# Kernel optimization log

Measured on AMD Instinct MI355X. Metric: run time of the kernel, lower is better.

Reference implementation:

```python
import jax, jax.numpy as jnp
import numpy as np

E, B, L, H1, H2, C = 8, 4096, 512, 1024, 512, 40


def setup_inputs() -> dict:
    key = jax.random.key(0)
    ks = jax.random.split(key, 9)
    return {
        "x_s": jax.random.normal(ks[0], (B, L), jnp.float32),
        "x_p": jax.random.normal(ks[1], (B, L), jnp.float32),
        "W1": jax.random.normal(ks[2], (E, 2 * L, H1), jnp.float32) / np.sqrt(2 * L).astype(np.float32),
        "b1": jax.random.normal(ks[3], (E, H1), jnp.float32) * 0.01,
        "W2": jax.random.normal(ks[4], (E, H1, H2), jnp.float32) / np.sqrt(H1).astype(np.float32),
        "b2": jax.random.normal(ks[5], (E, H2), jnp.float32) * 0.01,
        "W3": jax.random.normal(ks[6], (E, H2, C), jnp.float32) / np.sqrt(H2).astype(np.float32),
        "b3": jax.random.normal(ks[7], (E, C), jnp.float32) * 0.01,
        "sub_module_label": jax.random.randint(ks[8], (B,), 0, E, dtype=jnp.int32),
        "sub_id": 0,
    }


def reference(x_s, x_p, W1, b1, W2, b2, W3, b3, sub_module_label, sub_id):
    # Encoders (EEGNet/SCN/DCN) abstracted as identity: x_s / x_p are latent features.
    # Cls_HEAD.forward: x = cat([x_p, x_s], dim=1); per-sample routed 3-layer ELU MLP head.
    # Dropout is identity in eval mode.
    x = jnp.concatenate([x_p, x_s], axis=1)                      # [B, 2L]
    h = jax.nn.elu(jnp.einsum('bi,eih->ebh', x, W1) + b1[:, None, :])   # [E, B, H1]
    h = jax.nn.elu(jnp.einsum('ebh,ehk->ebk', h, W2) + b2[:, None, :])  # [E, B, H2]
    out_all = jnp.einsum('ebk,ekc->ebc', h, W3) + b3[:, None, :]        # [E, B, C]
    # select each sample's routed expert output
    bidx = jnp.arange(x.shape[0])
    return out_all[sub_module_label, bidx]                       # [B, C]
```

## Files before the change

kernel.cpp:

```cpp
#include <hip/hip_runtime.h>
#include <hip/hip_bf16.h>
#include <math.h>

#define En   8
#define Bn   4096
#define Ln   512
#define K1n  1024
#define H1n  1024
#define H2n  512
#define Cn   40
#define NP3  48
#define NTR  72

typedef unsigned short u16;
typedef __attribute__((ext_vector_type(8))) short bf16x8;
typedef __attribute__((ext_vector_type(4))) float f32x4;

__device__ __forceinline__ u16 f2b(float f) {
    union { float f; unsigned int u; } v; v.f = f;
    unsigned int r = v.u + 0x7FFF + ((v.u >> 16) & 1);
    return (u16)(r >> 16);
}

__device__ __forceinline__ void g2l16(const void* g, void* l) {
    __builtin_amdgcn_global_load_lds(
        (const __attribute__((address_space(1))) unsigned int*)(unsigned long long)g,
        (__attribute__((address_space(3))) unsigned int*)(unsigned int)(unsigned long long)l,
        16, 0, 0);
}

__device__ __forceinline__ void wtrans64(
    const float* __restrict__ Wsrc, u16* __restrict__ Wdst,
    int K, int N, int k0, int n0, int tid, float* sm )
{
    #pragma unroll
    for (int s = 0; s < 4; s++) {
        int idx = tid + s * 256;
        int kk = idx >> 4, c4 = (idx & 15) * 4;
        float4 v = *(const float4*)&Wsrc[(size_t)(k0 + kk) * N + n0 + c4];
        float* row = sm + kk * 65 + c4;
        row[0] = v.x; row[1] = v.y; row[2] = v.z; row[3] = v.w;
    }
    __syncthreads();
    #pragma unroll
    for (int s = 0; s < 4; s++) {
        int idx = tid + s * 256;
        int nn = idx >> 4, kc = (idx & 15) * 4;
        ushort4 o = make_ushort4(f2b(sm[(kc + 0) * 65 + nn]), f2b(sm[(kc + 1) * 65 + nn]),
                                 f2b(sm[(kc + 2) * 65 + nn]), f2b(sm[(kc + 3) * 65 + nn]));
        *(ushort4*)&Wdst[(size_t)(n0 + nn) * K + k0 + kc] = o;
    }
}

#define P1_TOT (1 + 256 + 2048)

__global__ __launch_bounds__(256) void prep1_kernel(
    const float* __restrict__ xs, const float* __restrict__ xp,
    const float* __restrict__ W1, const int* __restrict__ label,
    int* __restrict__ meta, int* __restrict__ perm,
    u16* __restrict__ Xb, u16* __restrict__ W1t)
{
    __shared__ __align__(16) float sm[64 * 65];
    const int bid = blockIdx.x;
    const int tid = threadIdx.x;

    if (bid == 0) {
        int* cnt = (int*)sm;
        int* off = cnt + En;
        if (tid < En) cnt[tid] = 0;
        __syncthreads();
        for (int b = tid; b < Bn; b += 256) atomicAdd(&cnt[label[b]], 1);
        __syncthreads();
        if (tid == 0) {
            int run = 0;
            for (int e = 0; e < En; e++) { off[e] = run; run += cnt[e]; }
            off[En] = run;
        }
        __syncthreads();
        if (tid < En) cnt[tid] = off[tid];
        __syncthreads();
        for (int b = tid; b < Bn; b += 256) {
            int e = label[b];
            perm[atomicAdd(&cnt[e], 1)] = b;
        }
        if (tid <= En) meta[tid] = off[tid];
    } else if (bid < 257) {
        int r0 = (bid - 1) * 16;
        #pragma unroll 4
        for (int s = 0; s < 16; s++) {
            int r = r0 + s;
            int k = tid * 4;
            const float* src = (k < Ln) ? (xp + (size_t)r * Ln + k)
                                        : (xs + (size_t)r * Ln + (k - Ln));
            float4 v = *(const float4*)src;
            *(ushort4*)&Xb[(size_t)r * K1n + k] =
                make_ushort4(f2b(v.x), f2b(v.y), f2b(v.z), f2b(v.w));
        }
    } else {
        int b = bid - 257;
        int e = b >> 8, rem = b & 255;
        int k0 = (rem >> 4) * 64, n0 = (rem & 15) * 64;
        wtrans64(W1 + (size_t)e * K1n * H1n, W1t + (size_t)e * H1n * K1n,
                 K1n, H1n, k0, n0, tid, sm);
    }
}

template <int K, int N, bool GATHER, bool FUSE3, bool PREP2>
__global__ __launch_bounds__(256) void mfma_gemm(
    const u16* __restrict__ A, const u16* __restrict__ Wt,
    const float* __restrict__ bias, const int* __restrict__ meta,
    const int* __restrict__ perm, u16* __restrict__ outb,
    const u16* __restrict__ Wt3, float* __restrict__ outf,
    const float* __restrict__ W2f, const float* __restrict__ W3f,
    const float* __restrict__ b3v, const int* __restrict__ labelv,
    u16* __restrict__ W2t_o, u16* __restrict__ W3t_o)
{
    constexpr int TM = 64, BK = 64;
    constexpr int T = K / BK;
    constexpr int NTC = N / 64;
    __shared__ __align__(16) u16 SM[16384];

    const int tid = threadIdx.x;
    const int bx = blockIdx.x;

    if (PREP2 && bx >= NTR * NTC) {
        int jb = bx - NTR * NTC;
        if (jb < 1024) {
            int e = jb >> 7, rem = jb & 127;
            int k0 = (rem >> 3) * 64, n0 = (rem & 7) * 64;
            wtrans64(W2f + (size_t)e * H1n * H2n, W2t_o + (size_t)e * H2n * H1n,
                     H1n, H2n, k0, n0, tid, (float*)SM);
        } else if (jb < 1024 + 128) {
            int b = jb - 1024;
            int e = b >> 4, k0 = (b & 15) * 32;
            const float* src = W3f + (size_t)e * H2n * Cn;
            u16* dst = W3t_o + (size_t)e * NP3 * H2n;
            float* t = (float*)SM;
            #pragma unroll
            for (int s = 0; s < 5; s++) {
                int idx = tid + s * 256;
                int kk = idx / Cn, nn = idx - kk * Cn;
                if (kk < 32) t[kk * 41 + nn] = src[(size_t)(k0 + kk) * Cn + nn];
            }
            __syncthreads();
            #pragma unroll
            for (int s = 0; s < 6; s++) {
                int idx = tid + s * 256;
                int nn = idx >> 5, kk = idx & 31;
                float v = (nn < Cn) ? t[kk * 41 + nn] : 0.f;
                dst[(size_t)nn * H2n + k0 + kk] = f2b(v);
            }
        } else {
            int b = jb - (1024 + 128);
            int r0 = b * 64;
            #pragma unroll
            for (int s = 0; s < 10; s++) {
                int idx = tid + s * 256;
                int r = r0 + idx / Cn;
                int c = idx - (idx / Cn) * Cn;
                outf[(size_t)r * Cn + c] = b3v[labelv[r] * Cn + c];
            }
        }
        return;
    }

    const int rt = bx % NTR;
    const int col0 = (bx / NTR) * 64;

    int expert = -1, row0 = 0, rowmax = 0, acc_t = 0;
    int prev = meta[0];
    #pragma unroll
    for (int e = 0; e < En; e++) {
        int nxt = meta[e + 1];
        int c = nxt - prev;
        int t = (c + TM - 1) / TM;
        if (expert < 0 && rt < acc_t + t) {
            expert = e; row0 = prev + (rt - acc_t) * TM; rowmax = nxt - 1;
        }
        acc_t += t; prev = nxt;
    }
    if (expert < 0) return;

    const u16* Wexp = Wt + (size_t)expert * N * K;

    const int lane = tid & 63;
    const int wid = tid >> 6;
    const int wm = (wid & 1) * 32;
    const int wn = (wid >> 1) * 32;
    const int l15 = lane & 15;
    const int lq = lane >> 4;

    const u16* aptr[2]; const u16* bptr[2];
    int aoff[2], boff[2];
    #pragma unroll
    for (int s = 0; s < 2; s++) {
        int idx = tid + s * 256;
        int rl = idx >> 3, c = idx & 7;
        int kq = c ^ (rl & 7);
        int rg = row0 + rl; if (rg > rowmax) rg = rowmax;
        if (GATHER) rg = perm[rg];
        aptr[s] = A + (size_t)rg * K + kq * 8;
        bptr[s] = Wexp + (size_t)(col0 + rl) * K + kq * 8;
        aoff[s] = idx * 8;
        boff[s] = 4096 + idx * 8;
    }
    const int csw = l15 & 7;

    f32x4 acc[2][2];
    #pragma unroll
    for (int i = 0; i < 2; i++)
        #pragma unroll
        for (int j = 0; j < 2; j++) acc[i][j] = (f32x4){0.f, 0.f, 0.f, 0.f};

    #pragma unroll
    for (int s = 0; s < 2; s++) {
        g2l16(aptr[s], &SM[aoff[s]]);
        g2l16(bptr[s], &SM[boff[s]]);
    }

    for (int t = 0; t < T; t++) {
        __syncthreads();
        const u16* As = &SM[(t & 1) * 8192];
        const u16* Bs = As + 4096;
        if (t + 1 < T) {
            int base = ((t + 1) & 1) * 8192;
            int ko = (t + 1) * BK;
            #pragma unroll
            for (int s = 0; s < 2; s++) {
                g2l16(aptr[s] + ko, &SM[base + aoff[s]]);
                g2l16(bptr[s] + ko, &SM[base + boff[s]]);
            }
        }
        #pragma unroll
        for (int h = 0; h < 2; h++) {
            const int ksw = ((h * 4 + lq) ^ csw) << 3;
            bf16x8 af[2], bf[2];
            #pragma unroll
            for (int i = 0; i < 2; i++)
                af[i] = *(const bf16x8*)&As[(wm + i * 16 + l15) * BK + ksw];
            #pragma unroll
            for (int j = 0; j < 2; j++)
                bf[j] = *(const bf16x8*)&Bs[(wn + j * 16 + l15) * BK + ksw];
            #pragma unroll
            for (int i = 0; i < 2; i++)
                #pragma unroll
                for (int j = 0; j < 2; j++)
                    acc[i][j] = __builtin_amdgcn_mfma_f32_16x16x32_bf16(
                        af[i], bf[j], acc[i][j], 0, 0, 0);
        }
    }

    if (!FUSE3) {
        #pragma unroll
        for (int i = 0; i < 2; i++) {
            #pragma unroll
            for (int j = 0; j < 2; j++) {
                int col = col0 + wn + j * 16 + l15;
                float bv = bias[expert * N + col];
                #pragma unroll
                for (int r = 0; r < 4; r++) {
                    int grow = row0 + wm + i * 16 + lq * 4 + r;
                    if (grow <= rowmax) {
                        float v = acc[i][j][r] + bv;
                        v = (v > 0.f) ? v : (expf(v) - 1.f);
                        outb[(size_t)grow * N + col] = f2b(v);
                    }
                }
            }
        }
    } else {
        __syncthreads();
        u16* H = &SM[0];
        #pragma unroll
        for (int i = 0; i < 2; i++) {
            #pragma unroll
            for (int j = 0; j < 2; j++) {
                int col = wn + j * 16 + l15;
                float bv = bias[expert * N + col0 + col];
                #pragma unroll
                for (int r = 0; r < 4; r++) {
                    float v = acc[i][j][r] + bv;
                    v = (v > 0.f) ? v : (expf(v) - 1.f);
                    H[(wm + i * 16 + lq * 4 + r) * 72 + col] = f2b(v);
                }
            }
        }
        __syncthreads();
        const int rh = wid * 16;
        f32x4 a3[3];
        #pragma unroll
        for (int j = 0; j < 3; j++) a3[j] = (f32x4){0.f, 0.f, 0.f, 0.f};
        #pragma unroll
        for (int ki = 0; ki < 2; ki++) {
            bf16x8 ha = *(const bf16x8*)&H[(rh + l15) * 72 + ki * 32 + lq * 8];
            #pragma unroll
            for (int j = 0; j < 3; j++) {
                bf16x8 wb = *(const bf16x8*)
                    &Wt3[((size_t)expert * NP3 + j * 16 + l15) * H2n + col0 + ki * 32 + lq * 8];
                a3[j] = __builtin_amdgcn_mfma_f32_16x16x32_bf16(ha, wb, a3[j], 0, 0, 0);
            }
        }
        #pragma unroll
        for (int j = 0; j < 3; j++) {
            int col = j * 16 + l15;
            if (col < Cn) {
                #pragma unroll
                for (int r = 0; r < 4; r++) {
                    int grow = row0 + rh + lq * 4 + r;
                    if (grow <= rowmax)
                        atomicAdd(&outf[(size_t)perm[grow] * Cn + col], a3[j][r]);
                }
            }
        }
    }
}

extern "C" void kernel_launch(void* const* d_in, const int* in_sizes, int n_in,
                              void* d_out, int out_size, void* d_ws, size_t ws_size,
                              hipStream_t stream)
{
    const float* xs = (const float*)d_in[0];
    const float* xp = (const float*)d_in[1];
    const float* W1 = (const float*)d_in[2];
    const float* b1 = (const float*)d_in[3];
    const float* W2 = (const float*)d_in[4];
    const float* b2 = (const float*)d_in[5];
    const float* W3 = (const float*)d_in[6];
    const float* b3 = (const float*)d_in[7];
    const int* label = (const int*)d_in[8];
    float* out = (float*)d_out;

    char* ws = (char*)d_ws;
    int* meta = (int*)ws;
    int* perm = (int*)(ws + 64);
    u16* Xb  = (u16*)(ws + (64 << 10));
    u16* W1t = (u16*)(ws + (64 << 10) + (8  << 20));
    u16* W2t = (u16*)(ws + (64 << 10) + (24 << 20));
    u16* h1b = (u16*)(ws + (64 << 10) + (32 << 20));
    u16* W3t = (u16*)(ws + (64 << 10) + (40 << 20));

    prep1_kernel<<<P1_TOT, 256, 0, stream>>>(
        xs, xp, W1, label, meta, perm, Xb, W1t);

    mfma_gemm<K1n, H1n, true, false, true><<<72 * 16 + 1216, 256, 0, stream>>>(
        Xb, W1t, b1, meta, perm, h1b, nullptr, out,
        W2, W3, b3, label, W2t, W3t);

    mfma_gemm<H1n, H2n, false, true, false><<<72 * 8, 256, 0, stream>>>(
        h1b, W2t, b2, meta, perm, nullptr, W3t, out,
        nullptr, nullptr, nullptr, nullptr, nullptr, nullptr);
}
```

Before: 172.1 us.

## Fuse fp32-to-bf16 conversion of X and W1 into first GEMM's load path

Removes the separate pass that converted X to bf16 and transposed W1 into bf16 scratch. The first GEMM now reads fp32 X rows (gathered via perm) and fp32 W1 directly, converting to bf16 in registers and writing into swizzled LDS with register prefetch double buffering. Routing becomes its own one-block kernel. This avoids writing and re-reading the bf16 copies. In exchange, each tile re-reads and re-converts the fp32 weights, doubling global bytes for W1 per tile. The synchronous register-staged loads also replace the async LDS loads that the GEMM used before.

Measured after the change: 187.6 us. 1.09x slower.

```diff
diff --git a/kernel.cpp b/kernel.cpp
--- a/kernel.cpp
+++ b/kernel.cpp
@@ -21,6 +21,12 @@
     unsigned int r = v.u + 0x7FFF + ((v.u >> 16) & 1);
     return (u16)(r >> 16);
 }
+__device__ __forceinline__ unsigned int f2b2(float a, float b) {
+    union { float f; unsigned int u; } x, y; x.f = a; y.f = b;
+    unsigned int ra = (x.u + 0x7FFF + ((x.u >> 16) & 1)) >> 16;
+    unsigned int rb = (y.u + 0x7FFF + ((y.u >> 16) & 1)) & 0xFFFF0000u;
+    return rb | ra;
+}
 
 __device__ __forceinline__ void g2l16(const void* g, void* l) {
     __builtin_amdgcn_global_load_lds(
@@ -31,7 +37,7 @@
 
 __device__ __forceinline__ void wtrans64(
     const float* __restrict__ Wsrc, u16* __restrict__ Wdst,
-    int K, int N, int k0, int n0, int tid, float* sm )
+    int K, int N, int k0, int n0, int tid, float* sm)
 {
     #pragma unroll
     for (int s = 0; s < 4; s++) {
@@ -52,78 +58,46 @@
     }
 }
 
-#define P1_TOT (1 + 256 + 2048)
-
-__global__ __launch_bounds__(256) void prep1_kernel(
-    const float* __restrict__ xs, const float* __restrict__ xp,
-    const float* __restrict__ W1, const int* __restrict__ label,
-    int* __restrict__ meta, int* __restrict__ perm,
-    u16* __restrict__ Xb, u16* __restrict__ W1t)
+__global__ __launch_bounds__(256) void route_kernel(
+    const int* __restrict__ label, int* __restrict__ meta, int* __restrict__ perm)
 {
-    __shared__ __align__(16) float sm[64 * 65];
-    const int bid = blockIdx.x;
+    __shared__ int cnt[En], off[En + 1];
     const int tid = threadIdx.x;
-
-    if (bid == 0) {
-        int* cnt = (int*)sm;
-        int* off = cnt + En;
-        if (tid < En) cnt[tid] = 0;
-        __syncthreads();
-        for (int b = tid; b < Bn; b += 256) atomicAdd(&cnt[label[b]], 1);
-        __syncthreads();
-        if (tid == 0) {
-            int run = 0;
-            for (int e = 0; e < En; e++) { off[e] = run; run += cnt[e]; }
-            off[En] = run;
-        }
-        __syncthreads();
-        if (tid < En) cnt[tid] = off[tid];
-        __syncthreads();
-        for (int b = tid; b < Bn; b += 256) {
-            int e = label[b];
-            perm[atomicAdd(&cnt[e], 1)] = b;
-        }
-        if (tid <= En) meta[tid] = off[tid];
-    } else if (bid < 257) {
-        int r0 = (bid - 1) * 16;
-        #pragma unroll 4
-        for (int s = 0; s < 16; s++) {
-            int r = r0 + s;
-            int k = tid * 4;
-            const float* src = (k < Ln) ? (xp + (size_t)r * Ln + k)
-                                        : (xs + (size_t)r * Ln + (k - Ln));
-            float4 v = *(const float4*)src;
-            *(ushort4*)&Xb[(size_t)r * K1n + k] =
-                make_ushort4(f2b(v.x), f2b(v.y), f2b(v.z), f2b(v.w));
-        }
-    } else {
-        int b = bid - 257;
-        int e = b >> 8, rem = b & 255;
-        int k0 = (rem >> 4) * 64, n0 = (rem & 15) * 64;
-        wtrans64(W1 + (size_t)e * K1n * H1n, W1t + (size_t)e * H1n * K1n,
-                 K1n, H1n, k0, n0, tid, sm);
-    }
-}
-
-template <int K, int N, bool GATHER, bool FUSE3, bool PREP2>
-__global__ __launch_bounds__(256) void mfma_gemm(
-    const u16* __restrict__ A, const u16* __restrict__ Wt,
-    const float* __restrict__ bias, const int* __restrict__ meta,
-    const int* __restrict__ perm, u16* __restrict__ outb,
-    const u16* __restrict__ Wt3, float* __restrict__ outf,
+    if (tid < En) cnt[tid] = 0;
+    __syncthreads();
+    for (int b = tid; b < Bn; b += 256) atomicAdd(&cnt[label[b]], 1);
+    __syncthreads();
+    if (tid == 0) {
+        int run = 0;
+        for (int e = 0; e < En; e++) { off[e] = run; run += cnt[e]; }
+        off[En] = run;
+    }
+    __syncthreads();
+    if (tid < En) cnt[tid] = off[tid];
+    __syncthreads();
+    for (int b = tid; b < Bn; b += 256) {
+        int e = label[b];
+        perm[atomicAdd(&cnt[e], 1)] = b;
+    }
+    if (tid <= En) meta[tid] = off[tid];
+}
+
+__global__ __launch_bounds__(256) void gemm1_kernel(
+    const float* __restrict__ xp, const float* __restrict__ xs,
+    const float* __restrict__ W1, const float* __restrict__ b1,
+    const int* __restrict__ meta, const int* __restrict__ perm,
+    u16* __restrict__ h1b,
     const float* __restrict__ W2f, const float* __restrict__ W3f,
     const float* __restrict__ b3v, const int* __restrict__ labelv,
-    u16* __restrict__ W2t_o, u16* __restrict__ W3t_o)
+    u16* __restrict__ W2t_o, u16* __restrict__ W3t_o, float* __restrict__ outf)
 {
-    constexpr int TM = 64, BK = 64;
-    constexpr int T = K / BK;
-    constexpr int NTC = N / 64;
+    constexpr int TM = 64, BK = 64, T = K1n / BK, NTC = H1n / 64;
     __shared__ __align__(16) u16 SM[16384];
 
     const int tid = threadIdx.x;
     const int bx = blockIdx.x;
 
-    if (PREP2 && bx >= NTR * NTC) {
+    if (bx >= NTR * NTC) {
         int jb = bx - NTR * NTC;
         if (jb < 1024) {
             int e = jb >> 7, rem = jb & 127;
@@ -181,8 +155,6 @@
     }
     if (expert < 0) return;
 
-    const u16* Wexp = Wt + (size_t)expert * N * K;
-
     const int lane = tid & 63;
     const int wid = tid >> 6;
     const int wm = (wid & 1) * 32;
@@ -190,6 +162,166 @@
     const int l15 = lane & 15;
     const int lq = lane >> 4;
 
+    const int rl = tid >> 2, lk2 = (tid & 3) * 2;
+    int rg = row0 + rl; if (rg > rowmax) rg = rowmax;
+    rg = perm[rg];
+    const float* axp = xp + (size_t)rg * Ln + lk2 * 8;
+    const float* axs = xs + (size_t)rg * Ln + lk2 * 8;
+    const int aslot0 = rl * 64 + (((lk2    ) ^ (rl & 7)) << 3);
+    const int aslot1 = rl * 64 + (((lk2 + 1) ^ (rl & 7)) << 3);
+
+    const int kg = tid >> 4;
+    const int n4 = (tid & 15) * 4;
+    const float* bbase = W1 + (size_t)expert * K1n * H1n + (size_t)(kg * 4) * H1n + col0 + n4;
+    int bslot[4];
+    #pragma unroll
+    for (int i = 0; i < 4; i++) {
+        int nl = n4 + i;
+        int sig = (nl ^ (nl >> 3)) & 7;
+        bslot[i] = 4096 + nl * 64 + ((((kg >> 1) ^ sig) << 3) + (kg & 1) * 4);
+    }
+
+    const int csw = l15 & 7;
+    int sB[2];
+    #pragma unroll
+    for (int j = 0; j < 2; j++) {
+        int nl = wn + j * 16 + l15;
+        sB[j] = (nl ^ (nl >> 3)) & 7;
+    }
+
+    f32x4 acc[2][2];
+    #pragma unroll
+    for (int i = 0; i < 2; i++)
+        #pragma unroll
+        for (int j = 0; j < 2; j++) acc[i][j] = (f32x4){0.f, 0.f, 0.f, 0.f};
+
+    {
+        const float* ap = axp;
+        float4 av0 = *(const float4*)(ap + 0),  av1 = *(const float4*)(ap + 4);
+        float4 av2 = *(const float4*)(ap + 8),  av3 = *(const float4*)(ap + 12);
+        float4 wv[4];
+        #pragma unroll
+        for (int d = 0; d < 4; d++) wv[d] = *(const float4*)(bbase + (size_t)d * H1n);
+        *(uint4*)&SM[aslot0] = make_uint4(f2b2(av0.x, av0.y), f2b2(av0.z, av0.w),
+                                          f2b2(av1.x, av1.y), f2b2(av1.z, av1.w));
+        *(uint4*)&SM[aslot1] = make_uint4(f2b2(av2.x, av2.y), f2b2(av2.z, av2.w),
+                                          f2b2(av3.x, av3.y), f2b2(av3.z, av3.w));
+        #pragma unroll
+        for (int i = 0; i < 4; i++) {
+            float c0 = ((const float*)&wv[0])[i], c1 = ((const float*)&wv[1])[i];
+            float c2 = ((const float*)&wv[2])[i], c3 = ((const float*)&wv[3])[i];
+            *(uint2*)&SM[bslot[i]] = make_uint2(f2b2(c0, c1), f2b2(c2, c3));
+        }
+    }
+
+    for (int t = 0; t < T; t++) {
+        __syncthreads();
+        const u16* As = &SM[(t & 1) * 8192];
+        const u16* Bs = As + 4096;
+        u16* Sn = &SM[((t + 1) & 1) * 8192];
+
+        float4 av0, av1, av2, av3, wv[4];
+        const bool pf = (t + 1 < T);
+        if (pf) {
+            const int tn = t + 1;
+            const float* ap = (tn < 8) ? (axp + tn * 64) : (axs + (tn - 8) * 64);
+            av0 = *(const float4*)(ap + 0);  av1 = *(const float4*)(ap + 4);
+            av2 = *(const float4*)(ap + 8);  av3 = *(const float4*)(ap + 12);
+            const float* bp = bbase + (size_t)tn * 64 * H1n;
+            #pragma unroll
+            for (int d = 0; d < 4; d++) wv[d] = *(const float4*)(bp + (size_t)d * H1n);
+        }
+
+        #pragma unroll
+        for (int h = 0; h < 2; h++) {
+            const int ksA = ((h * 4 + lq) ^ csw) << 3;
+            bf16x8 af[2], bf[2];
+            #pragma unroll
+            for (int i = 0; i < 2; i++)
+                af[i] = *(const bf16x8*)&As[(wm + i * 16 + l15) * 64 + ksA];
+            #pragma unroll
+            for (int j = 0; j < 2; j++)
+                bf[j] = *(const bf16x8*)&Bs[(wn + j * 16 + l15) * 64 +
+                                            (((h * 4 + lq) ^ sB[j]) << 3)];
+            #pragma unroll
+            for (int i = 0; i < 2; i++)
+                #pragma unroll
+                for (int j = 0; j < 2; j++)
+                    acc[i][j] = __builtin_amdgcn_mfma_f32_16x16x32_bf16(
+                        af[i], bf[j], acc[i][j], 0, 0, 0);
+        }
+
+        if (pf) {
+            *(uint4*)&Sn[aslot0] = make_uint4(f2b2(av0.x, av0.y), f2b2(av0.z, av0.w),
+                                              f2b2(av1.x, av1.y), f2b2(av1.z, av1.w));
+            *(uint4*)&Sn[aslot1] = make_uint4(f2b2(av2.x, av2.y), f2b2(av2.z, av2.w),
+                                              f2b2(av3.x, av3.y), f2b2(av3.z, av3.w));
+            #pragma unroll
+            for (int i = 0; i < 4; i++) {
+                float c0 = ((const float*)&wv[0])[i], c1 = ((const float*)&wv[1])[i];
+                float c2 = ((const float*)&wv[2])[i], c3 = ((const float*)&wv[3])[i];
+                *(uint2*)&Sn[bslot[i]] = make_uint2(f2b2(c0, c1), f2b2(c2, c3));
+            }
+        }
+    }
+
+    #pragma unroll
+    for (int i = 0; i < 2; i++) {
+        #pragma unroll
+        for (int j = 0; j < 2; j++) {
+            int col = col0 + wn + j * 16 + l15;
+            float bv = b1[expert * H1n + col];
+            #pragma unroll
+            for (int r = 0; r < 4; r++) {
+                int grow = row0 + wm + i * 16 + lq * 4 + r;
+                if (grow <= rowmax) {
+                    float v = acc[i][j][r] + bv;
+                    v = (v > 0.f) ? v : (expf(v) - 1.f);
+                    h1b[(size_t)grow * H1n + col] = f2b(v);
+                }
+            }
+        }
+    }
+}
+
+__global__ __launch_bounds__(256) void gemm2_kernel(
+    const u16* __restrict__ A, const u16* __restrict__ Wt,
+    const float* __restrict__ bias, const int* __restrict__ meta,
+    const int* __restrict__ perm, const u16* __restrict__ Wt3,
+    float* __restrict__ outf)
+{
+    constexpr int TM = 64, BK = 64, K = H1n, N = H2n, T = K / BK;
+    __shared__ __align__(16) u16 SM[16384];
+
+    const int tid = threadIdx.x;
+    const int bx = blockIdx.x;
+
+    const int rt = bx % NTR;
+    const int col0 = (bx / NTR) * 64;
+
+    int expert = -1, row0 = 0, rowmax = 0, acc_t = 0;
+    int prev = meta[0];
+    #pragma unroll
+    for (int e = 0; e < En; e++) {
+        int nxt = meta[e + 1];
+        int c = nxt - prev;
+        int t = (c + TM - 1) / TM;
+        if (expert < 0 && rt < acc_t + t) {
+            expert = e; row0 = prev + (rt - acc_t) * TM; rowmax = nxt - 1;
+        }
+        acc_t += t; prev = nxt;
+    }
+    if (expert < 0) return;
+
+    const u16* Wexp = Wt + (size_t)expert * N * K;
+
+    const int lane = tid & 63;
+    const int wid = tid >> 6;
+    const int wm = (wid & 1) * 32;
+    const int wn = (wid >> 1) * 32;
+    const int l15 = lane & 15;
+    const int lq = lane >> 4;
+
     const u16* aptr[2]; const u16* bptr[2];
     int aoff[2], boff[2];
     #pragma unroll
@@ -198,7 +330,6 @@
         int rl = idx >> 3, c = idx & 7;
         int kq = c ^ (rl & 7);
         int rg = row0 + rl; if (rg > rowmax) rg = rowmax;
-        if (GATHER) rg = perm[rg];
         aptr[s] = A + (size_t)rg * K + kq * 8;
         bptr[s] = Wexp + (size_t)(col0 + rl) * K + kq * 8;
         aoff[s] = idx * 8;
@@ -250,66 +381,46 @@
         }
     }
 
-    if (!FUSE3) {
-        #pragma unroll
-        for (int i = 0; i < 2; i++) {
-            #pragma unroll
-            for (int j = 0; j < 2; j++) {
-                int col = col0 + wn + j * 16 + l15;
-                float bv = bias[expert * N + col];
-                #pragma unroll
-                for (int r = 0; r < 4; r++) {
-                    int grow = row0 + wm + i * 16 + lq * 4 + r;
-                    if (grow <= rowmax) {
-                        float v = acc[i][j][r] + bv;
-                        v = (v > 0.f) ? v : (expf(v) - 1.f);
-                        outb[(size_t)grow * N + col] = f2b(v);
-                    }
-                }
-            }
-        }
-    } else {
-        __syncthreads();
-        u16* H = &SM[0];
-        #pragma unroll
-        for (int i = 0; i < 2; i++) {
-            #pragma unroll
-            for (int j = 0; j < 2; j++) {
-                int col = wn + j * 16 + l15;
-                float bv = bias[expert * N + col0 + col];
-                #pragma unroll
-                for (int r = 0; r < 4; r++) {
-                    float v = acc[i][j][r] + bv;
-                    v = (v > 0.f) ? v : (expf(v) - 1.f);
-                    H[(wm + i * 16 + lq * 4 + r) * 72 + col] = f2b(v);
-                }
-            }
-        }
-        __syncthreads();
-        const int rh = wid * 16;
-        f32x4 a3[3];
-        #pragma unroll
-        for (int j = 0; j < 3; j++) a3[j] = (f32x4){0.f, 0.f, 0.f, 0.f};
-        #pragma unroll
-        for (int ki = 0; ki < 2; ki++) {
-            bf16x8 ha = *(const bf16x8*)&H[(rh + l15) * 72 + ki * 32 + lq * 8];
-            #pragma unroll
-            for (int j = 0; j < 3; j++) {
-                bf16x8 wb = *(const bf16x8*)
-                    &Wt3[((size_t)expert * NP3 + j * 16 + l15) * H2n + col0 + ki * 32 + lq * 8];
-                a3[j] = __builtin_amdgcn_mfma_f32_16x16x32_bf16(ha, wb, a3[j], 0, 0, 0);
-            }
-        }
+    __syncthreads();
+    u16* H = &SM[0];
+    #pragma unroll
+    for (int i = 0; i < 2; i++) {
+        #pragma unroll
+        for (int j = 0; j < 2; j++) {
+            int col = wn + j * 16 + l15;
+            float bv = bias[expert * N + col0 + col];
+            #pragma unroll
+            for (int r = 0; r < 4; r++) {
+                float v = acc[i][j][r] + bv;
+                v = (v > 0.f) ? v : (expf(v) - 1.f);
+                H[(wm + i * 16 + lq * 4 + r) * 72 + col] = f2b(v);
+            }
+        }
+    }
+    __syncthreads();
+    const int rh = wid * 16;
+    f32x4 a3[3];
+    #pragma unroll
+    for (int j = 0; j < 3; j++) a3[j] = (f32x4){0.f, 0.f, 0.f, 0.f};
+    #pragma unroll
+    for (int ki = 0; ki < 2; ki++) {
+        bf16x8 ha = *(const bf16x8*)&H[(rh + l15) * 72 + ki * 32 + lq * 8];
         #pragma unroll
         for (int j = 0; j < 3; j++) {
-            int col = j * 16 + l15;
-            if (col < Cn) {
-                #pragma unroll
-                for (int r = 0; r < 4; r++) {
-                    int grow = row0 + rh + lq * 4 + r;
-                    if (grow <= rowmax)
-                        atomicAdd(&outf[(size_t)perm[grow] * Cn + col], a3[j][r]);
-                }
+            bf16x8 wb = *(const bf16x8*)
+                &Wt3[((size_t)expert * NP3 + j * 16 + l15) * H2n + col0 + ki * 32 + lq * 8];
+            a3[j] = __builtin_amdgcn_mfma_f32_16x16x32_bf16(ha, wb, a3[j], 0, 0, 0);
+        }
+    }
+    #pragma unroll
+    for (int j = 0; j < 3; j++) {
+        int col = j * 16 + l15;
+        if (col < Cn) {
+            #pragma unroll
+            for (int r = 0; r < 4; r++) {
+                int grow = row0 + rh + lq * 4 + r;
+                if (grow <= rowmax)
+                    atomicAdd(&outf[(size_t)perm[grow] * Cn + col], a3[j][r]);
             }
         }
     }
@@ -333,20 +444,15 @@
     char* ws = (char*)d_ws;
     int* meta = (int*)ws;
     int* perm = (int*)(ws + 64);
-    u16* Xb  = (u16*)(ws + (64 << 10));
-    u16* W1t = (u16*)(ws + (64 << 10) + (8  << 20));
-    u16* W2t = (u16*)(ws + (64 << 10) + (24 << 20));
-    u16* h1b = (u16*)(ws + (64 << 10) + (32 << 20));
-    u16* W3t = (u16*)(ws + (64 << 10) + (40 << 20));
-
-    prep1_kernel<<<P1_TOT, 256, 0, stream>>>(
-        xs, xp, W1, label, meta, perm, Xb, W1t);
-
-    mfma_gemm<K1n, H1n, true, false, true><<<72 * 16 + 1216, 256, 0, stream>>>(
-        Xb, W1t, b1, meta, perm, h1b, nullptr, out,
-        W2, W3, b3, label, W2t, W3t);
-
-    mfma_gemm<H1n, H2n, false, true, false><<<72 * 8, 256, 0, stream>>>(
-        h1b, W2t, b2, meta, perm, nullptr, W3t, out,
-        nullptr, nullptr, nullptr, nullptr, nullptr, nullptr);
-}
+    u16* h1b = (u16*)(ws + (64 << 10));
+    u16* W2t = (u16*)(ws + (64 << 10) + (8 << 20));
+    u16* W3t = (u16*)(ws + (64 << 10) + (16 << 20));
+
+    route_kernel<<<1, 256, 0, stream>>>(label, meta, perm);
+
+    gemm1_kernel<<<NTR * 16 + 1216, 256, 0, stream>>>(
+        xp, xs, W1, b1, meta, perm, h1b, W2, W3, b3, label, W2t, W3t, out);
+
+    gemm2_kernel<<<NTR * 8, 256, 0, stream>>>(
+        h1b, W2t, b2, meta, perm, W3t, out);
+}
```
